# Optimization experiments

Measured on AMD Instinct MI355X. Metric: run time of the kernel, lower is better.

The kernel has to match this reference:

```python
import jax, jax.numpy as jnp
import numpy as np

B = 16          # number of sequences
L = 2048        # tokens per sequence (uniform here; math handles ragged)
D = 4096        # hidden size (GritLM-7B)
TOTAL = B * L   # flattened total tokens
EPS = 1e-12     # torch F.normalize eps (PoolerHead normalize=True)


def setup_inputs() -> dict:
    key = jax.random.key(0)
    k1, k2 = jax.random.split(key)
    hidden_states = jax.random.normal(k1, (TOTAL, D), dtype=jnp.float32)
    prompt_lens = jnp.full((B,), L, dtype=jnp.int32)          # sum == TOTAL
    instruction_lens = jax.random.randint(k2, (B,), 1, 33, dtype=jnp.int32)
    return {
        "hidden_states": hidden_states,
        "prompt_lens": prompt_lens,
        "instruction_lens": instruction_lens,
    }


def reference(hidden_states, prompt_lens, instruction_lens):
    # hidden_states: [total_tokens, D]; prompt_lens/instruction_lens: [B]
    n = hidden_states.shape[0]
    ends = jnp.cumsum(prompt_lens)          # [B] exclusive segment ends
    starts = ends - prompt_lens             # [B] segment starts
    pos = jnp.arange(n)
    seg = jnp.searchsorted(ends, pos, side="right")  # [total] segment id per token
    pos_in_seg = pos - starts[seg]
    # mask out the first instruction_len tokens of each sequence
    mask = pos_in_seg >= instruction_lens[seg]
    masked = jnp.where(mask[:, None], hidden_states, jnp.zeros((), hidden_states.dtype))
    sums = jax.ops.segment_sum(masked, seg, num_segments=prompt_lens.shape[0])  # [B, D]
    counts = (prompt_lens - instruction_lens).astype(hidden_states.dtype)        # [B]
    mean = sums / counts[:, None]
    # PoolerHead(normalize=True): L2 normalize per sequence
    norm = jnp.maximum(jnp.linalg.norm(mean, axis=-1, keepdims=True), EPS)
    return mean / norm
```

## Files before the change

### kernel.cpp

```cpp
#include <hip/hip_runtime.h>
#include <math.h>

#define TPB 256

__global__ void __launch_bounds__(TPB) grit_partial_kernel(
    const float* __restrict__ hs,
    const int* __restrict__ plens,
    const int* __restrict__ ilens,
    float* __restrict__ sums,
    int B, int D, int n_row_chunks)
{
    const int b = blockIdx.z;
    const int plen = plens[b];
    const int ilen = ilens[b];

    int start = 0;
    for (int i = 0; i < b; ++i) start += plens[i];

    const int rpc = (plen + n_row_chunks - 1) / n_row_chunks;
    int r_lo = blockIdx.y * rpc;
    int r_hi = r_lo + rpc;
    if (r_hi > plen) r_hi = plen;
    if (r_lo < ilen) r_lo = ilen;
    if (r_lo >= r_hi) return;

    const int col = (blockIdx.x * TPB + threadIdx.x) * 4;
    if (col >= D) return;

    const float* __restrict__ base = hs + (size_t)start * (size_t)D + col;

    float4 acc = make_float4(0.f, 0.f, 0.f, 0.f);
    for (int r = r_lo; r < r_hi; ++r) {
        const float4 v = *(const float4*)(base + (size_t)r * (size_t)D);
        acc.x += v.x;
        acc.y += v.y;
        acc.z += v.z;
        acc.w += v.w;
    }

    float* dst = sums + (size_t)b * (size_t)D + col;
    atomicAdd(dst + 0, acc.x);
    atomicAdd(dst + 1, acc.y);
    atomicAdd(dst + 2, acc.z);
    atomicAdd(dst + 3, acc.w);
}

__global__ void __launch_bounds__(TPB) grit_finalize_kernel(
    const int* __restrict__ plens,
    const int* __restrict__ ilens,
    const float* __restrict__ sums,
    float* __restrict__ out,
    int D)
{
    const int b = blockIdx.x;
    const float cnt = (float)(plens[b] - ilens[b]);
    const float inv = 1.0f / cnt;

    const float* __restrict__ s = sums + (size_t)b * (size_t)D;
    float* __restrict__ o = out + (size_t)b * (size_t)D;

    float sq = 0.f;
    for (int col = threadIdx.x * 4; col < D; col += TPB * 4) {
        const float4 v = *(const float4*)(s + col);
        const float mx = v.x * inv, my = v.y * inv, mz = v.z * inv, mw = v.w * inv;
        sq += mx * mx + my * my + mz * mz + mw * mw;
    }

    #pragma unroll
    for (int off = 32; off > 0; off >>= 1)
        sq += __shfl_down(sq, off, 64);

    __shared__ float wsum[TPB / 64];
    const int lane = threadIdx.x & 63;
    const int wave = threadIdx.x >> 6;
    if (lane == 0) wsum[wave] = sq;
    __syncthreads();

    float total = 0.f;
    #pragma unroll
    for (int w = 0; w < TPB / 64; ++w) total += wsum[w];

    float norm = sqrtf(total);
    norm = fmaxf(norm, 1e-12f);
    const float invn = inv / norm;

    for (int col = threadIdx.x * 4; col < D; col += TPB * 4) {
        const float4 v = *(const float4*)(s + col);
        float4 r;
        r.x = v.x * invn;
        r.y = v.y * invn;
        r.z = v.z * invn;
        r.w = v.w * invn;
        *(float4*)(o + col) = r;
    }
}

extern "C" void kernel_launch(void* const* d_in, const int* in_sizes, int n_in,
                              void* d_out, int out_size, void* d_ws, size_t ws_size,
                              hipStream_t stream) {
    const float* hs    = (const float*)d_in[0];
    const int*   plens = (const int*)d_in[1];
    const int*   ilens = (const int*)d_in[2];
    float*       out   = (float*)d_out;

    const int B = in_sizes[1];
    const int D = out_size / B;

    float* sums = (float*)d_ws;

    hipMemsetAsync(sums, 0, (size_t)B * (size_t)D * sizeof(float), stream);

    const int n_row_chunks = 32;
    const int col_chunks = (D + TPB * 4 - 1) / (TPB * 4);
    dim3 grid(col_chunks, n_row_chunks, B);
    grit_partial_kernel<<<grid, TPB, 0, stream>>>(hs, plens, ilens, sums,
                                                  B, D, n_row_chunks);

    grit_finalize_kernel<<<B, TPB, 0, stream>>>(plens, ilens, sums, out, D);
}
```

Before: 701.4 us.

## Unroll row accumulation and replace atomics with per-chunk partial sums

The partial kernel now loads four rows per iteration into independent accumulators, which raises memory-level parallelism in the main streaming loop. The memset and atomicAdd reduction are replaced by writing per-row-chunk partials to workspace. The finalize kernel then reduces the 32 partials per column, stores the mean, and rescales it in place. This removes the memset launch and atomics but needs a larger workspace and makes the 16-block finalize read more data.

```diff
diff --git a/kernel.cpp b/kernel.cpp
--- a/kernel.cpp
+++ b/kernel.cpp
@@ -2,68 +2,91 @@
 #include <math.h>
 
 #define TPB 256
+#define ROW_CHUNKS 32
 
 __global__ void __launch_bounds__(TPB) grit_partial_kernel(
     const float* __restrict__ hs,
     const int* __restrict__ plens,
     const int* __restrict__ ilens,
-    float* __restrict__ sums,
-    int B, int D, int n_row_chunks)
+    float* __restrict__ partials,
+    int B, int D)
 {
-    const int b = blockIdx.z;
+    const int b  = blockIdx.z;
+    const int ry = blockIdx.y;
     const int plen = plens[b];
     const int ilen = ilens[b];
 
     int start = 0;
     for (int i = 0; i < b; ++i) start += plens[i];
 
-    const int rpc = (plen + n_row_chunks - 1) / n_row_chunks;
-    int r_lo = blockIdx.y * rpc;
+    const int rpc = (plen + ROW_CHUNKS - 1) / ROW_CHUNKS;
+    int r_lo = ry * rpc;
     int r_hi = r_lo + rpc;
     if (r_hi > plen) r_hi = plen;
     if (r_lo < ilen) r_lo = ilen;
-    if (r_lo >= r_hi) return;
 
     const int col = (blockIdx.x * TPB + threadIdx.x) * 4;
     if (col >= D) return;
 
-    const float* __restrict__ base = hs + (size_t)start * (size_t)D + col;
+    float4 a0 = make_float4(0.f, 0.f, 0.f, 0.f);
+    float4 a1 = a0, a2 = a0, a3 = a0;
 
-    float4 acc = make_float4(0.f, 0.f, 0.f, 0.f);
-    for (int r = r_lo; r < r_hi; ++r) {
-        const float4 v = *(const float4*)(base + (size_t)r * (size_t)D);
-        acc.x += v.x;
-        acc.y += v.y;
-        acc.z += v.z;
-        acc.w += v.w;
+    if (r_lo < r_hi) {
+        const size_t stride = (size_t)D * sizeof(float);
+        const char* p = (const char*)(hs + (size_t)(start + r_lo) * (size_t)D + col);
+        int r = r_lo;
+        for (; r + 4 <= r_hi; r += 4) {
+            const float4 v0 = *(const float4*)(p);
+            const float4 v1 = *(const float4*)(p + stride);
+            const float4 v2 = *(const float4*)(p + 2 * stride);
+            const float4 v3 = *(const float4*)(p + 3 * stride);
+            p += 4 * stride;
+            a0.x += v0.x; a0.y += v0.y; a0.z += v0.z; a0.w += v0.w;
+            a1.x += v1.x; a1.y += v1.y; a1.z += v1.z; a1.w += v1.w;
+            a2.x += v2.x; a2.y += v2.y; a2.z += v2.z; a2.w += v2.w;
+            a3.x += v3.x; a3.y += v3.y; a3.z += v3.z; a3.w += v3.w;
+        }
+        for (; r < r_hi; ++r) {
+            const float4 v = *(const float4*)(p);
+            p += stride;
+            a0.x += v.x; a0.y += v.y; a0.z += v.z; a0.w += v.w;
+        }
     }
 
-    float* dst = sums + (size_t)b * (size_t)D + col;
-    atomicAdd(dst + 0, acc.x);
-    atomicAdd(dst + 1, acc.y);
-    atomicAdd(dst + 2, acc.z);
-    atomicAdd(dst + 3, acc.w);
+    float4 t;
+    t.x = (a0.x + a1.x) + (a2.x + a3.x);
+    t.y = (a0.y + a1.y) + (a2.y + a3.y);
+    t.z = (a0.z + a1.z) + (a2.z + a3.z);
+    t.w = (a0.w + a1.w) + (a2.w + a3.w);
+
+    *(float4*)(partials + (size_t)(b * ROW_CHUNKS + ry) * (size_t)D + col) = t;
 }
 
 __global__ void __launch_bounds__(TPB) grit_finalize_kernel(
     const int* __restrict__ plens,
     const int* __restrict__ ilens,
-    const float* __restrict__ sums,
+    const float* __restrict__ partials,
     float* __restrict__ out,
     int D)
 {
     const int b = blockIdx.x;
-    const float cnt = (float)(plens[b] - ilens[b]);
-    const float inv = 1.0f / cnt;
+    const float inv = 1.0f / (float)(plens[b] - ilens[b]);
 
-    const float* __restrict__ s = sums + (size_t)b * (size_t)D;
+    const float* __restrict__ p = partials + (size_t)b * ROW_CHUNKS * (size_t)D;
     float* __restrict__ o = out + (size_t)b * (size_t)D;
 
     float sq = 0.f;
     for (int col = threadIdx.x * 4; col < D; col += TPB * 4) {
-        const float4 v = *(const float4*)(s + col);
-        const float mx = v.x * inv, my = v.y * inv, mz = v.z * inv, mw = v.w * inv;
-        sq += mx * mx + my * my + mz * mz + mw * mw;
+        float4 s = make_float4(0.f, 0.f, 0.f, 0.f);
+        #pragma unroll
+        for (int ry = 0; ry < ROW_CHUNKS; ++ry) {
+            const float4 v = *(const float4*)(p + (size_t)ry * (size_t)D + col);
+            s.x += v.x; s.y += v.y; s.z += v.z; s.w += v.w;
+        }
+        float4 m;
+        m.x = s.x * inv; m.y = s.y * inv; m.z = s.z * inv; m.w = s.w * inv;
+        sq += m.x * m.x + m.y * m.y + m.z * m.z + m.w * m.w;
+        *(float4*)(o + col) = m;
     }
 
     #pragma unroll
@@ -80,17 +103,12 @@
     #pragma unroll
     for (int w = 0; w < TPB / 64; ++w) total += wsum[w];
 
-    float norm = sqrtf(total);
-    norm = fmaxf(norm, 1e-12f);
-    const float invn = inv / norm;
+    const float invn = 1.0f / fmaxf(sqrtf(total), 1e-12f);
 
     for (int col = threadIdx.x * 4; col < D; col += TPB * 4) {
-        const float4 v = *(const float4*)(s + col);
+        const float4 m = *(const float4*)(o + col);
         float4 r;
-        r.x = v.x * invn;
-        r.y = v.y * invn;
-        r.z = v.z * invn;
-        r.w = v.w * invn;
+        r.x = m.x * invn; r.y = m.y * invn; r.z = m.z * invn; r.w = m.w * invn;
         *(float4*)(o + col) = r;
     }
 }
@@ -106,15 +124,11 @@
     const int B = in_sizes[1];
     const int D = out_size / B;
 
-    float* sums = (float*)d_ws;
+    float* partials = (float*)d_ws;
 
-    hipMemsetAsync(sums, 0, (size_t)B * (size_t)D * sizeof(float), stream);
+    const int col_chunks = (D + TPB * 4 - 1) / (TPB * 4);
+    dim3 grid(col_chunks, ROW_CHUNKS, B);
+    grit_partial_kernel<<<grid, TPB, 0, stream>>>(hs, plens, ilens, partials, B, D);
 
-    const int n_row_chunks = 32;
-    const int col_chunks = (D + TPB * 4 - 1) / (TPB * 4);
-    dim3 grid(col_chunks, n_row_chunks, B);
-    grit_partial_kernel<<<grid, TPB, 0, stream>>>(hs, plens, ilens, sums,
-                                                  B, D, n_row_chunks);
-
-    grit_finalize_kernel<<<B, TPB, 0, stream>>>(plens, ilens, sums, out, D);
+    grit_finalize_kernel<<<B, TPB, 0, stream>>>(plens, ilens, partials, out, D);
 }
```

After: 676.8 us. 3.5% less time.
